# Optimization experiments

Measured on AMD Instinct MI355X. Metric: run time of the kernel, lower is better.

Reference implementation:

```python
import jax, jax.numpy as jnp
import numpy as np

HID = 50  # HIDDEN_SIZE in source


def _lstm_step(x, h, c, W_ih, W_hh, b):
    # PyTorch LSTM cell: gates order i, f, g, o
    gates = x @ W_ih.T + h @ W_hh.T + b  # [B, 4H]
    i, f, g, o = jnp.split(gates, 4, axis=-1)
    i = jax.nn.sigmoid(i)
    f = jax.nn.sigmoid(f)
    g = jnp.tanh(g)
    o = jax.nn.sigmoid(o)
    c = f * c + i * g
    h = o * jnp.tanh(c)
    return h, c


def setup_inputs() -> dict:
    key = jax.random.key(0)
    ks = jax.random.split(key, 11)
    B, S = 2048, 512
    H, I, O = HID, 1, 1
    s = 1.0 / np.sqrt(H)
    u = lambda k, shp: jax.random.uniform(k, shp, jnp.float32, -s, s)
    return {
        "source": jax.random.normal(ks[0], (B, S, I), jnp.float32),
        "enc_W_ih": u(ks[1], (4 * H, I)),
        "enc_W_hh": u(ks[2], (4 * H, H)),
        "enc_b_ih": u(ks[3], (4 * H,)),
        "enc_b_hh": u(ks[4], (4 * H,)),
        "dec_W_ih": u(ks[5], (4 * H, O)),
        "dec_W_hh": u(ks[6], (4 * H, H)),
        "dec_b_ih": u(ks[7], (4 * H,)),
        "dec_b_hh": u(ks[8], (4 * H,)),
        "fc_W": u(ks[9], (O, H)),
        "fc_b": u(ks[10], (O,)),
        "target_len": 256,
    }


def reference(source, enc_W_ih, enc_W_hh, enc_b_ih, enc_b_hh,
              dec_W_ih, dec_W_hh, dec_b_ih, dec_b_hh, fc_W, fc_b,
              target_len):
    B = source.shape[0]
    H = enc_W_hh.shape[1]
    dt = source.dtype
    h0 = jnp.zeros((B, H), dt)
    c0 = jnp.zeros((B, H), dt)

    enc_b = enc_b_ih + enc_b_hh

    def enc_step(carry, x_t):
        h, c = carry
        h, c = _lstm_step(x_t, h, c, enc_W_ih, enc_W_hh, enc_b)
        return (h, c), None

    # scan over time: [S, B, 1]
    (h, c), _ = jax.lax.scan(enc_step, (h0, c0), jnp.swapaxes(source, 0, 1))

    dec_b = dec_b_ih + dec_b_hh
    x0 = jnp.zeros((B, source.shape[2]), dt)  # decoder_input = zeros

    def dec_step(carry, _):
        x, h, c = carry
        h, c = _lstm_step(x, h, c, dec_W_ih, dec_W_hh, dec_b)
        y = h @ fc_W.T + fc_b  # [B, 1]
        return (y, h, c), y  # feed output back as next input

    _, ys = jax.lax.scan(dec_step, (x0, h, c), None, length=target_len)
    return jnp.swapaxes(ys, 0, 1)  # [B, target_len, 1]
```

## Files before the change

kernel.cpp:

```cpp
#include <hip/hip_runtime.h>


#define HID 50
#define SEQ 512
#define TGT 256
#define MB  8
#define L2E 1.44269504088896341f

typedef __attribute__((ext_vector_type(8))) short short8;
typedef __attribute__((ext_vector_type(4))) float f32x4;

__device__ __forceinline__ unsigned short f2bf(float f) {
    unsigned u = __float_as_uint(f);
    return (unsigned short)((u + 0x7fffu + ((u >> 16) & 1u)) >> 16);
}
__device__ __forceinline__ float bf2f(unsigned short b) {
    return __uint_as_float(((unsigned)b) << 16);
}
__device__ __forceinline__ float sigm2(float a) {
    return __builtin_amdgcn_rcpf(1.0f + __builtin_amdgcn_exp2f(-a));
}
__device__ __forceinline__ float tanhc(float c) {
    return fmaf(2.0f,
        __builtin_amdgcn_rcpf(1.0f + __builtin_amdgcn_exp2f(-2.0f * L2E * c)),
        -1.0f);
}

#define MFMA(A, B, C) __builtin_amdgcn_mfma_f32_16x16x32_bf16((A), (B), (C), 0, 0, 0)

#define HBLK 72
#define HFB(s, kt, qg) ((((s) * 2 + (kt)) * 4 + (qg)) * HBLK)
#define HFSZ (2 * 2 * 4 * HBLK)

#define GCORE(X4, HIN, HOUT)                                           \
    float hv0, hv1;                                                    \
    {                                                                  \
        const short* hin_ = (HIN);                                     \
        short8 a00 = *(const short8*)(hin_ + HFB(0, 0, kg) + (lane & 7) * 8); \
        short8 a01 = *(const short8*)(hin_ + HFB(1, 0, kg) + (lane & 7) * 8); \
        short8 a10 = *(const short8*)(hin_ + HFB(0, 1, kg) + (lane & 7) * 8); \
        short8 a11 = *(const short8*)(hin_ + HFB(1, 1, kg) + (lane & 7) * 8); \
        f32x4 ac0, ac1, ac2, ac3;                                      \
        _Pragma("unroll")                                              \
        for (int r = 0; r < 4; ++r) {                                  \
            ac0[r] = fmaf(wx[0], (X4)[r], bb[0]);                      \
            ac1[r] = fmaf(wx[1], (X4)[r], bb[1]);                      \
            ac2[r] = fmaf(wx[2], (X4)[r], bb[2]);                      \
            ac3[r] = fmaf(wx[3], (X4)[r], bb[3]);                      \
        }                                                              \
        ac0 = MFMA(a00, Bf[0][0][0], ac0);                             \
        ac1 = MFMA(a00, Bf[1][0][0], ac1);                             \
        ac2 = MFMA(a00, Bf[2][0][0], ac2);                             \
        ac3 = MFMA(a00, Bf[3][0][0], ac3);                             \
        ac0 = MFMA(a00, Bf[0][0][1], ac0);                             \
        ac1 = MFMA(a00, Bf[1][0][1], ac1);                             \
        ac2 = MFMA(a00, Bf[2][0][1], ac2);                             \
        ac3 = MFMA(a00, Bf[3][0][1], ac3);                             \
        ac0 = MFMA(a01, Bf[0][0][0], ac0);                             \
        ac1 = MFMA(a01, Bf[1][0][0], ac1);                             \
        ac2 = MFMA(a01, Bf[2][0][0], ac2);                             \
        ac3 = MFMA(a01, Bf[3][0][0], ac3);                             \
        ac0 = MFMA(a10, Bf[0][1][0], ac0);                             \
        ac1 = MFMA(a10, Bf[1][1][0], ac1);                             \
        ac2 = MFMA(a10, Bf[2][1][0], ac2);                             \
        ac3 = MFMA(a10, Bf[3][1][0], ac3);                             \
        ac0 = MFMA(a10, Bf[0][1][1], ac0);                             \
        ac1 = MFMA(a10, Bf[1][1][1], ac1);                             \
        ac2 = MFMA(a10, Bf[2][1][1], ac2);                             \
        ac3 = MFMA(a10, Bf[3][1][1], ac3);                             \
        ac0 = MFMA(a11, Bf[0][1][0], ac0);                             \
        ac1 = MFMA(a11, Bf[1][1][0], ac1);                             \
        ac2 = MFMA(a11, Bf[2][1][0], ac2);                             \
        ac3 = MFMA(a11, Bf[3][1][0], ac3);                             \
        const bool hi_ = (kg & 2);    \
        float gi0 = hi_ ? ac0[2] : ac0[0], gi1 = hi_ ? ac0[3] : ac0[1]; \
        float gf0 = hi_ ? ac1[2] : ac1[0], gf1 = hi_ ? ac1[3] : ac1[1]; \
        float gg0 = hi_ ? ac2[2] : ac2[0], gg1 = hi_ ? ac2[3] : ac2[1]; \
        float go0 = hi_ ? ac3[2] : ac3[0], go1 = hi_ ? ac3[3] : ac3[1]; \
        float vi0 = sigm2(gi0), vi1 = sigm2(gi1);                      \
        float vf0 = sigm2(gf0), vf1 = sigm2(gf1);                      \
        float vg0 = fmaf(2.0f, sigm2(gg0), -1.0f);                     \
        float vg1 = fmaf(2.0f, sigm2(gg1), -1.0f);                     \
        float vo0 = sigm2(go0), vo1 = sigm2(go1);                      \
        cc0 = fmaf(vf0, cc0, vi0 * vg0);                               \
        cc1 = fmaf(vf1, cc1, vi1 * vg1);                               \
        hv0 = vo0 * tanhc(cc0);                                        \
        hv1 = vo1 * tanhc(cc1);                                        \
        short* ho_ = (HOUT);                                           \
        unsigned short q0 = f2bf(hv0);                                 \
        unsigned short q1 = f2bf(hv0 - bf2f(q0));                      \
        unsigned short q2 = f2bf(hv1);                                 \
        unsigned short q3 = f2bf(hv1 - bf2f(q2));                      \
        ho_[wr00] = (short)q0;  ho_[wr01] = (short)q1;                 \
        ho_[wr10] = (short)q2;  ho_[wr11] = (short)q3;                 \
    }

#define DSTEP(T, HIN, HOUT, PB)                                        \
    {                                                                  \
        GCORE(xc, HIN, HOUT)                                           \
        float p0 = fcw * hv0, p1 = fcw * hv1;                          \
        p0 += __shfl_xor(p0, 1, 64);  p1 += __shfl_xor(p1, 1, 64);     \
        p0 += __shfl_xor(p0, 2, 64);  p1 += __shfl_xor(p1, 2, 64);     \
        p0 += __shfl_xor(p0, 4, 64);  p1 += __shfl_xor(p1, 4, 64);     \
        p0 += __shfl_xor(p0, 8, 64);  p1 += __shfl_xor(p1, 8, 64);     \
        if (nl == 0) { (PB)[e0 * 4 + w] = p0; (PB)[e0 * 4 + 4 + w] = p1; } \
        __syncthreads();                                               \
        f32x4 s0_ = *(const f32x4*)&(PB)[e0 * 4];                      \
        f32x4 s1_ = *(const f32x4*)&(PB)[e0 * 4 + 4];                  \
        float y0 = s0_[0] + s0_[1] + s0_[2] + s0_[3] + fb;             \
        float y1 = s1_[0] + s1_[1] + s1_[2] + s1_[3] + fb;             \
        if (w == 0 && nl == 0) {                                       \
            out[(size_t)(b0 + e0) * TGT + (T)] = y0;                   \
            out[(size_t)(b0 + e0 + 1) * TGT + (T)] = y1;               \
        }                                                              \
        float yp0 = __shfl_xor(y0, 32, 64);                            \
        float yp1 = __shfl_xor(y1, 32, 64);                            \
        xc = (kg < 2) ? (f32x4){y0, y1, yp0, yp1}                      \
                      : (f32x4){yp0, yp1, y0, y1};                     \
    }

extern "C" __global__ void __launch_bounds__(256, 1)
seq2seq_kernel(const float* __restrict__ src,
               const float* __restrict__ eWih, const float* __restrict__ eWhh,
               const float* __restrict__ eBih, const float* __restrict__ eBhh,
               const float* __restrict__ dWih, const float* __restrict__ dWhh,
               const float* __restrict__ dBih, const float* __restrict__ dBhh,
               const float* __restrict__ fcW, const float* __restrict__ fcB,
               float* __restrict__ out) {
    const int tid  = threadIdx.x;
    const int lane = tid & 63;
    const int w    = tid >> 6;
    const int nl   = lane & 15;
    const int kg   = lane >> 4;
    const int un   = 16 * w + nl;
    const int b0   = blockIdx.x * MB;
    const int e0   = 4 * (kg & 1) + 2 * (kg >> 1);
    const int ukt  = un >> 5, uqg = (un >> 3) & 3, uj = un & 7;
    const int wr00 = HFB(0, ukt, uqg) + e0 * 8 + uj;
    const int wr01 = HFB(1, ukt, uqg) + e0 * 8 + uj;
    const int wr10 = wr00 + 8;
    const int wr11 = wr01 + 8;

    __shared__ __align__(16) short hfA[HFSZ], hfB[HFSZ];
    __shared__ __align__(16) float srcT[SEQ * MB];
    __shared__ __align__(16) float pbA[64], pbB[64];

    for (int i = tid; i < HFSZ; i += 256) { hfA[i] = 0; hfB[i] = 0; }
    for (int i = tid; i < SEQ * MB; i += 256) {
        int e = i >> 9, t = i & 511;
        srcT[t * MB + e] = src[(size_t)(b0 + e) * SEQ + t];
    }

    short8 Bf[4][2][2];
    float bb[4], wx[4];
    float cc0 = 0.0f, cc1 = 0.0f;

    auto loadW = [&](const float* Wih, const float* Whh,
                     const float* Bih, const float* Bhh) {
#pragma unroll
        for (int g = 0; g < 4; ++g) {
            const float sc = (g == 2) ? 2.0f * L2E : L2E;
            const bool nv  = (un < HID);
            const int row  = g * HID + (nv ? un : 0);
            bb[g] = nv ? (Bih[row] + Bhh[row]) * sc : 0.0f;
            wx[g] = nv ? Wih[row] * sc : 0.0f;
#pragma unroll
            for (int kt = 0; kt < 2; ++kt) {
                short8 s0, s1;
#pragma unroll
                for (int j = 0; j < 8; ++j) {
                    int kk = kt * 32 + kg * 8 + j;
                    float wv = (nv && kk < HID)
                             ? Whh[(size_t)row * HID + kk] * sc : 0.0f;
                    unsigned short h0 = f2bf(wv);
                    unsigned short h1 = f2bf(wv - bf2f(h0));
                    s0[j] = (short)h0; s1[j] = (short)h1;
                }
                Bf[g][kt][0] = s0; Bf[g][kt][1] = s1;
            }
        }
    };

    loadW(eWih, eWhh, eBih, eBhh);
    __syncthreads();
    for (int t = 0; t < SEQ; t += 2) {
        {
            f32x4 xe = *(const f32x4*)&srcT[t * MB + 4 * (kg & 1)];
            GCORE(xe, hfA, hfB)
        }
        __syncthreads();
        {
            f32x4 xe = *(const f32x4*)&srcT[(t + 1) * MB + 4 * (kg & 1)];
            GCORE(xe, hfB, hfA)
        }
        __syncthreads();
    }

    loadW(dWih, dWhh, dBih, dBhh);
    const float fcw = (un < HID) ? fcW[un] : 0.0f;
    const float fb  = fcB[0];
    f32x4 xc = {0.f, 0.f, 0.f, 0.f};
    for (int t = 0; t < TGT; t += 2) {
        DSTEP(t,     hfA, hfB, pbA)
        DSTEP(t + 1, hfB, hfA, pbB)
    }
}

extern "C" void kernel_launch(void* const* d_in, const int* in_sizes, int n_in,
                              void* d_out, int out_size, void* d_ws, size_t ws_size,
                              hipStream_t stream) {
    const float* src  = (const float*)d_in[0];
    const float* eWih = (const float*)d_in[1];
    const float* eWhh = (const float*)d_in[2];
    const float* eBih = (const float*)d_in[3];
    const float* eBhh = (const float*)d_in[4];
    const float* dWih = (const float*)d_in[5];
    const float* dWhh = (const float*)d_in[6];
    const float* dBih = (const float*)d_in[7];
    const float* dBhh = (const float*)d_in[8];
    const float* fcW  = (const float*)d_in[9];
    const float* fcB  = (const float*)d_in[10];
    float* out = (float*)d_out;

    const int B = in_sizes[0] / SEQ;
    seq2seq_kernel<<<B / MB, 256, 0, stream>>>(src, eWih, eWhh, eBih, eBhh,
                                               dWih, dWhh, dBih, dBhh,
                                               fcW, fcB, out);
}
```

Before: 551.5 us.

## Halve batch rows per block and run two LSTM blocks per CU

```diff
diff --git a/kernel.cpp b/kernel.cpp
--- a/kernel.cpp
+++ b/kernel.cpp
@@ -4,7 +4,7 @@
 #define HID 50
 #define SEQ 512
 #define TGT 256
-#define MB  8
+#define MB  4
 #define L2E 1.44269504088896341f
 
 typedef __attribute__((ext_vector_type(8))) short short8;
@@ -28,26 +28,25 @@
 
 #define MFMA(A, B, C) __builtin_amdgcn_mfma_f32_16x16x32_bf16((A), (B), (C), 0, 0, 0)
 
-#define HBLK 72
-#define HFB(s, kt, qg) ((((s) * 2 + (kt)) * 4 + (qg)) * HBLK)
-#define HFSZ (2 * 2 * 4 * HBLK)
-
-#define GCORE(X4, HIN, HOUT)                                           \
-    float hv0, hv1;                                                    \
+#define HB(s, kt, qg) ((((s) * 2 + (kt)) * 4 + (qg)) * 32)
+#define HFSZ (2 * 2 * 4 * 32)
+
+#define GCORE(XK, HIN, HOUT)                                           \
+    float hv;                                                          \
     {                                                                  \
         const short* hin_ = (HIN);                                     \
-        short8 a00 = *(const short8*)(hin_ + HFB(0, 0, kg) + (lane & 7) * 8); \
-        short8 a01 = *(const short8*)(hin_ + HFB(1, 0, kg) + (lane & 7) * 8); \
-        short8 a10 = *(const short8*)(hin_ + HFB(0, 1, kg) + (lane & 7) * 8); \
-        short8 a11 = *(const short8*)(hin_ + HFB(1, 1, kg) + (lane & 7) * 8); \
-        f32x4 ac0, ac1, ac2, ac3;                                      \
-        _Pragma("unroll")                                              \
-        for (int r = 0; r < 4; ++r) {                                  \
-            ac0[r] = fmaf(wx[0], (X4)[r], bb[0]);                      \
-            ac1[r] = fmaf(wx[1], (X4)[r], bb[1]);                      \
-            ac2[r] = fmaf(wx[2], (X4)[r], bb[2]);                      \
-            ac3[r] = fmaf(wx[3], (X4)[r], bb[3]);                      \
-        }                                                              \
+        short8 a00 = *(const short8*)(hin_ + HB(0, 0, kg) + bsel * 8); \
+        short8 a01 = *(const short8*)(hin_ + HB(1, 0, kg) + bsel * 8); \
+        short8 a10 = *(const short8*)(hin_ + HB(0, 1, kg) + bsel * 8); \
+        short8 a11 = *(const short8*)(hin_ + HB(1, 1, kg) + bsel * 8); \
+        float i0 = fmaf(wx[0], (XK), bb[0]);                           \
+        float i1 = fmaf(wx[1], (XK), bb[1]);                           \
+        float i2 = fmaf(wx[2], (XK), bb[2]);                           \
+        float i3 = fmaf(wx[3], (XK), bb[3]);                           \
+        f32x4 ac0 = {i0, i0, i0, i0};                                  \
+        f32x4 ac1 = {i1, i1, i1, i1};                                  \
+        f32x4 ac2 = {i2, i2, i2, i2};                                  \
+        f32x4 ac3 = {i3, i3, i3, i3};                                  \
         ac0 = MFMA(a00, Bf[0][0][0], ac0);                             \
         ac1 = MFMA(a00, Bf[1][0][0], ac1);                             \
         ac2 = MFMA(a00, Bf[2][0][0], ac2);                             \
@@ -72,54 +71,36 @@
         ac1 = MFMA(a11, Bf[1][1][0], ac1);                             \
         ac2 = MFMA(a11, Bf[2][1][0], ac2);                             \
         ac3 = MFMA(a11, Bf[3][1][0], ac3);                             \
-        const bool hi_ = (kg & 2);    \
-        float gi0 = hi_ ? ac0[2] : ac0[0], gi1 = hi_ ? ac0[3] : ac0[1]; \
-        float gf0 = hi_ ? ac1[2] : ac1[0], gf1 = hi_ ? ac1[3] : ac1[1]; \
-        float gg0 = hi_ ? ac2[2] : ac2[0], gg1 = hi_ ? ac2[3] : ac2[1]; \
-        float go0 = hi_ ? ac3[2] : ac3[0], go1 = hi_ ? ac3[3] : ac3[1]; \
-        float vi0 = sigm2(gi0), vi1 = sigm2(gi1);                      \
-        float vf0 = sigm2(gf0), vf1 = sigm2(gf1);                      \
-        float vg0 = fmaf(2.0f, sigm2(gg0), -1.0f);                     \
-        float vg1 = fmaf(2.0f, sigm2(gg1), -1.0f);                     \
-        float vo0 = sigm2(go0), vo1 = sigm2(go1);                      \
-        cc0 = fmaf(vf0, cc0, vi0 * vg0);                               \
-        cc1 = fmaf(vf1, cc1, vi1 * vg1);                               \
-        hv0 = vo0 * tanhc(cc0);                                        \
-        hv1 = vo1 * tanhc(cc1);                                        \
+        float vi = sigm2(ac0[0]);                                      \
+        float vf = sigm2(ac1[0]);                                      \
+        float vg = fmaf(2.0f, sigm2(ac2[0]), -1.0f);                   \
+        float vo = sigm2(ac3[0]);                                      \
+        cc = fmaf(vf, cc, vi * vg);                                    \
+        hv = vo * tanhc(cc);                                           \
+        unsigned short q0 = f2bf(hv);                                  \
+        unsigned short q1 = f2bf(hv - bf2f(q0));                       \
         short* ho_ = (HOUT);                                           \
-        unsigned short q0 = f2bf(hv0);                                 \
-        unsigned short q1 = f2bf(hv0 - bf2f(q0));                      \
-        unsigned short q2 = f2bf(hv1);                                 \
-        unsigned short q3 = f2bf(hv1 - bf2f(q2));                      \
-        ho_[wr00] = (short)q0;  ho_[wr01] = (short)q1;                 \
-        ho_[wr10] = (short)q2;  ho_[wr11] = (short)q3;                 \
+        ho_[wr0] = (short)q0;                                          \
+        ho_[wr1] = (short)q1;                                          \
     }
 
 #define DSTEP(T, HIN, HOUT, PB)                                        \
     {                                                                  \
         GCORE(xc, HIN, HOUT)                                           \
-        float p0 = fcw * hv0, p1 = fcw * hv1;                          \
-        p0 += __shfl_xor(p0, 1, 64);  p1 += __shfl_xor(p1, 1, 64);     \
-        p0 += __shfl_xor(p0, 2, 64);  p1 += __shfl_xor(p1, 2, 64);     \
-        p0 += __shfl_xor(p0, 4, 64);  p1 += __shfl_xor(p1, 4, 64);     \
-        p0 += __shfl_xor(p0, 8, 64);  p1 += __shfl_xor(p1, 8, 64);     \
-        if (nl == 0) { (PB)[e0 * 4 + w] = p0; (PB)[e0 * 4 + 4 + w] = p1; } \
+        float p = fcw * hv;                                            \
+        p += __shfl_xor(p, 1, 64);                                     \
+        p += __shfl_xor(p, 2, 64);                                     \
+        p += __shfl_xor(p, 4, 64);                                     \
+        p += __shfl_xor(p, 8, 64);                                     \
+        if (nl == 0) (PB)[kg * 4 + w] = p;                             \
         __syncthreads();                                               \
-        f32x4 s0_ = *(const f32x4*)&(PB)[e0 * 4];                      \
-        f32x4 s1_ = *(const f32x4*)&(PB)[e0 * 4 + 4];                  \
-        float y0 = s0_[0] + s0_[1] + s0_[2] + s0_[3] + fb;             \
-        float y1 = s1_[0] + s1_[1] + s1_[2] + s1_[3] + fb;             \
-        if (w == 0 && nl == 0) {                                       \
-            out[(size_t)(b0 + e0) * TGT + (T)] = y0;                   \
-            out[(size_t)(b0 + e0 + 1) * TGT + (T)] = y1;               \
-        }                                                              \
-        float yp0 = __shfl_xor(y0, 32, 64);                            \
-        float yp1 = __shfl_xor(y1, 32, 64);                            \
-        xc = (kg < 2) ? (f32x4){y0, y1, yp0, yp1}                      \
-                      : (f32x4){yp0, yp1, y0, y1};                     \
-    }
-
-extern "C" __global__ void __launch_bounds__(256, 1)
+        f32x4 s_ = *(const f32x4*)&(PB)[kg * 4];                       \
+        float y = s_[0] + s_[1] + s_[2] + s_[3] + fb;                  \
+        if (w == 0 && nl == 0) out[(size_t)(b0 + kg) * TGT + (T)] = y; \
+        xc = y;                                                        \
+    }
+
+extern "C" __global__ void __launch_bounds__(256, 2)
 seq2seq_kernel(const float* __restrict__ src,
                const float* __restrict__ eWih, const float* __restrict__ eWhh,
                const float* __restrict__ eBih, const float* __restrict__ eBhh,
@@ -132,18 +113,16 @@
     const int w    = tid >> 6;
     const int nl   = lane & 15;
     const int kg   = lane >> 4;
+    const int bsel = nl >> 2;
     const int un   = 16 * w + nl;
     const int b0   = blockIdx.x * MB;
-    const int e0   = 4 * (kg & 1) + 2 * (kg >> 1);
     const int ukt  = un >> 5, uqg = (un >> 3) & 3, uj = un & 7;
-    const int wr00 = HFB(0, ukt, uqg) + e0 * 8 + uj;
-    const int wr01 = HFB(1, ukt, uqg) + e0 * 8 + uj;
-    const int wr10 = wr00 + 8;
-    const int wr11 = wr01 + 8;
+    const int wr0  = HB(0, ukt, uqg) + kg * 8 + uj;
+    const int wr1  = HB(1, ukt, uqg) + kg * 8 + uj;
 
     __shared__ __align__(16) short hfA[HFSZ], hfB[HFSZ];
     __shared__ __align__(16) float srcT[SEQ * MB];
-    __shared__ __align__(16) float pbA[64], pbB[64];
+    __shared__ __align__(16) float pbA[16], pbB[16];
 
     for (int i = tid; i < HFSZ; i += 256) { hfA[i] = 0; hfB[i] = 0; }
     for (int i = tid; i < SEQ * MB; i += 256) {
@@ -153,7 +132,7 @@
 
     short8 Bf[4][2][2];
     float bb[4], wx[4];
-    float cc0 = 0.0f, cc1 = 0.0f;
+    float cc = 0.0f;
 
     auto loadW = [&](const float* Wih, const float* Whh,
                      const float* Bih, const float* Bhh) {
@@ -184,22 +163,16 @@
     loadW(eWih, eWhh, eBih, eBhh);
     __syncthreads();
     for (int t = 0; t < SEQ; t += 2) {
-        {
-            f32x4 xe = *(const f32x4*)&srcT[t * MB + 4 * (kg & 1)];
-            GCORE(xe, hfA, hfB)
-        }
+        { GCORE(srcT[t * MB + kg], hfA, hfB) }
         __syncthreads();
-        {
-            f32x4 xe = *(const f32x4*)&srcT[(t + 1) * MB + 4 * (kg & 1)];
-            GCORE(xe, hfB, hfA)
-        }
+        { GCORE(srcT[(t + 1) * MB + kg], hfB, hfA) }
         __syncthreads();
     }
 
     loadW(dWih, dWhh, dBih, dBhh);
     const float fcw = (un < HID) ? fcW[un] : 0.0f;
     const float fb  = fcB[0];
-    f32x4 xc = {0.f, 0.f, 0.f, 0.f};
+    float xc = 0.0f;
     for (int t = 0; t < TGT; t += 2) {
         DSTEP(t,     hfA, hfB, pbA)
         DSTEP(t + 1, hfB, hfA, pbB)
```

After: 530.8 us. -3.8%, faster.
